# Performance work log

Hardware: AMD Instinct MI355X
Metric: run time of the kernel (lower is better)

Reference implementation:

```python
import jax, jax.numpy as jnp
import numpy as np

N, E, C = 50000, 10000, 500
NNZ = 400000
IN_DIM, EDGE_DIM, NODE_DIM, COMP_DIM = 128, 128, 128, 128


def _glorot(key, shape):
    fan = shape[0] + shape[1]
    return jax.random.normal(key, shape, jnp.float32) * (2.0 / fan) ** 0.5


def _seg_mean(vals, idx, num):
    # mean aggregation over segments (scatter-add + count normalize)
    s = jax.ops.segment_sum(vals, idx, num_segments=num)
    cnt = jax.ops.segment_sum(jnp.ones((idx.shape[0], 1), vals.dtype), idx, num_segments=num)
    return s / jnp.maximum(cnt, 1.0)


def _prelu(v, a):
    return jnp.where(v >= 0, v, a * v)


def _conv(x, ni, ei, ec_e, ec_c, nc_n, nc_c, n_nodes, n_edges, n_comps,
          Wne, Wen, Wec, Wnc, a):
    # node -> hyperedge message passing
    e = _seg_mean((x @ Wne)[ni], ei, n_edges)            # [E, edge_dim]
    e_act = _prelu(e, a)
    # hyperedge -> node
    n = _seg_mean((e_act @ Wen)[ei], ni, n_nodes)        # [N, node_dim]
    # edge -> component and node -> component
    c = _seg_mean((e_act @ Wec)[ec_e], ec_c, n_comps) + \
        _seg_mean((x @ Wnc)[nc_n], nc_c, n_comps)        # [C, comp_dim]
    return n, e, c


def setup_inputs() -> dict:
    key = jax.random.key(0)
    ks = jax.random.split(key, 16)
    x = jax.random.normal(ks[0], (N, IN_DIM), jnp.float32)
    hyperedge_index = jnp.stack([
        jax.random.randint(ks[1], (NNZ,), 0, N),
        jax.random.randint(ks[2], (NNZ,), 0, E),
    ])
    hyperedge_component_index = jnp.stack([
        jnp.arange(E), jax.random.randint(ks[3], (E,), 0, C)])
    node_component_index = jnp.stack([
        jnp.arange(N), jax.random.randint(ks[4], (N,), 0, C)])
    return dict(
        x=x,
        hyperedge_index=hyperedge_index,
        hyperedge_component_index=hyperedge_component_index,
        node_component_index=node_component_index,
        num_nodes=N, num_edges=E, num_components=C,
        W_ne0=_glorot(ks[5], (IN_DIM, EDGE_DIM)),
        W_en0=_glorot(ks[6], (EDGE_DIM, NODE_DIM)),
        W_ec0=_glorot(ks[7], (EDGE_DIM, COMP_DIM)),
        W_nc0=_glorot(ks[8], (IN_DIM, COMP_DIM)),
        W_ne1=_glorot(ks[9], (NODE_DIM, EDGE_DIM)),
        W_en1=_glorot(ks[10], (EDGE_DIM, NODE_DIM)),
        W_ec1=_glorot(ks[11], (EDGE_DIM, COMP_DIM)),
        W_nc1=_glorot(ks[12], (NODE_DIM, COMP_DIM)),
        prelu_a=jnp.array(0.25, jnp.float32),
    )


def reference(x, hyperedge_index, hyperedge_component_index, node_component_index,
              num_nodes, num_edges, num_components,
              W_ne0, W_en0, W_ec0, W_nc0, W_ne1, W_en1, W_ec1, W_nc1, prelu_a):
    ni, ei = hyperedge_index[0], hyperedge_index[1]
    ec_e, ec_c = hyperedge_component_index[0], hyperedge_component_index[1]
    nc_n, nc_c = node_component_index[0], node_component_index[1]
    layers = [(W_ne0, W_en0, W_ec0, W_nc0), (W_ne1, W_en1, W_ec1, W_nc1)]
    e_out = c_out = None
    for Wne, Wen, Wec, Wnc in layers:
        n_out, e_out, c_out = _conv(x, ni, ei, ec_e, ec_c, nc_n, nc_c,
                                    num_nodes, num_edges, num_components,
                                    Wne, Wen, Wec, Wnc, prelu_a)
        x = _prelu(n_out, prelu_a)  # HyperEncoder applies act between/after layers
    return (x, e_out, c_out)
```

## Files before the change

### kernel.cpp

```cpp
#include <hip/hip_runtime.h>
#include <stdint.h>

typedef unsigned int u32;
typedef _Float16 f16;
typedef f16 half8 __attribute__((ext_vector_type(8)));
typedef float f32x4 __attribute__((ext_vector_type(4)));
#define TS 4096
#define KB2 256
#define CH 2048

__device__ __forceinline__ float bflo(u32 u) { return __uint_as_float(u << 16); }
__device__ __forceinline__ float bfhi(u32 u) { return __uint_as_float(u & 0xffff0000u); }
__device__ __forceinline__ u32 f2bf(float x) {
    u32 u = __float_as_uint(x);
    return (u + 0x7fffu + ((u >> 16) & 1u)) >> 16;
}
__device__ __forceinline__ u32 pack2(float a, float b) { return f2bf(a) | (f2bf(b) << 16); }

__device__ __forceinline__ int bstart2(int b, int total) {
    return (int)(((unsigned long long)b * (u32)total + KB2 - 1) / KB2);
}

__device__ __forceinline__ int blk_exscan(int v, int& total) {
    __shared__ int ws[5];
    int t = threadIdx.x, lane = t & 63, w = t >> 6;
    int inc = v;
    for (int d = 1; d < 64; d <<= 1) { int u = __shfl_up(inc, d, 64); if (lane >= d) inc += u; }
    __syncthreads();
    if (lane == 63) ws[w] = inc;
    __syncthreads();
    if (t == 0) { int acc = 0; for (int i = 0; i < 4; ++i) { int x = ws[i]; ws[i] = acc; acc += x; } ws[4] = acc; }
    __syncthreads();
    total = ws[4];
    return ws[w] + (inc - v);
}

#define ACC8(v) do { \
    a[0] += bflo((v).x); a[1] += bfhi((v).x); a[2] += bflo((v).y); a[3] += bfhi((v).y); \
    a[4] += bflo((v).z); a[5] += bfhi((v).z); a[6] += bflo((v).w); a[7] += bfhi((v).w); } while (0)

__device__ __forceinline__ void seg_mean8(const u32* __restrict__ in,
                                          const int* __restrict__ items,
                                          const int* __restrict__ off,
                                          int nseg, int nrows, int seg, float a[8]) {
    int lane = threadIdx.x & 63;
    int rs = lane >> 4;
    int cc = lane & 15;
#pragma unroll
    for (int i = 0; i < 8; ++i) a[i] = 0.f;
    int s0 = 0, s1 = 0;
    if (seg < nseg) { s0 = off[seg]; s1 = off[seg + 1]; }
    const uint4* rows = (const uint4*)in;
    int base = s0;
    for (; base + 16 <= s1; base += 16) {
        u32 r0 = (u32)items[base + rs];
        u32 r1 = (u32)items[base + 4 + rs];
        u32 r2 = (u32)items[base + 8 + rs];
        u32 r3 = (u32)items[base + 12 + rs];
        r0 = (r0 < (u32)nrows) ? r0 : 0u;
        r1 = (r1 < (u32)nrows) ? r1 : 0u;
        r2 = (r2 < (u32)nrows) ? r2 : 0u;
        r3 = (r3 < (u32)nrows) ? r3 : 0u;
        uint4 v0 = rows[(size_t)r0 * 16 + cc];
        uint4 v1 = rows[(size_t)r1 * 16 + cc];
        uint4 v2 = rows[(size_t)r2 * 16 + cc];
        uint4 v3 = rows[(size_t)r3 * 16 + cc];
        ACC8(v0); ACC8(v1); ACC8(v2); ACC8(v3);
    }
    for (; base + 8 <= s1; base += 8) {
        u32 r0 = (u32)items[base + rs];
        u32 r1 = (u32)items[base + 4 + rs];
        r0 = (r0 < (u32)nrows) ? r0 : 0u;
        r1 = (r1 < (u32)nrows) ? r1 : 0u;
        uint4 v0 = rows[(size_t)r0 * 16 + cc];
        uint4 v1 = rows[(size_t)r1 * 16 + cc];
        ACC8(v0); ACC8(v1);
    }
    int idx = base + rs;
    if (idx < s1) {
        u32 r = (u32)items[idx]; r = (r < (u32)nrows) ? r : 0u;
        uint4 v = rows[(size_t)r * 16 + cc];
        ACC8(v);
    }
    idx += 4;
    if (idx < s1) {
        u32 r = (u32)items[idx]; r = (r < (u32)nrows) ? r : 0u;
        uint4 v = rows[(size_t)r * 16 + cc];
        ACC8(v);
    }
#pragma unroll
    for (int i = 0; i < 8; ++i) {
        a[i] += __shfl_xor(a[i], 16, 64);
        a[i] += __shfl_xor(a[i], 32, 64);
    }
    float inv = 1.f / fmaxf((float)(s1 - s0), 1.f);
#pragma unroll
    for (int i = 0; i < 8; ++i) a[i] *= inv;
}

__device__ __forceinline__ void agg4_body(const u32* __restrict__ in,
                                          const int* __restrict__ items,
                                          const int* __restrict__ off,
                                          float* __restrict__ out_f32,
                                          u32* __restrict__ out_bf,
                                          int nseg, int nrows, int do_prelu,
                                          const float* __restrict__ alpha_p, int seg) {
    if (seg >= nseg) return;
    int lane = threadIdx.x & 63;
    int rs = lane >> 4;
    int cc = lane & 15;
    float a[8];
    seg_mean8(in, items, off, nseg, nrows, seg, a);
    if (do_prelu) {
        float al = *alpha_p;
#pragma unroll
        for (int i = 0; i < 8; ++i) a[i] = (a[i] >= 0.f) ? a[i] : al * a[i];
    }
    if (rs == 0) {
        if (out_f32) {
            float* o = out_f32 + ((size_t)seg << 7) + cc * 8;
            *(float4*)o       = make_float4(a[0], a[1], a[2], a[3]);
            *(float4*)(o + 4) = make_float4(a[4], a[5], a[6], a[7]);
        }
        if (out_bf) {
            uint4 pk;
            pk.x = pack2(a[0], a[1]); pk.y = pack2(a[2], a[3]);
            pk.z = pack2(a[4], a[5]); pk.w = pack2(a[6], a[7]);
            *(uint4*)(out_bf + ((size_t)seg << 6) + cc * 4) = pk;
        }
    }
}

__global__ __launch_bounds__(256) void k_front(
        const int* __restrict__ ni, const int* __restrict__ ei,
        const int* __restrict__ nc_c, const int* __restrict__ ec_c,
        int* __restrict__ bcntE, int* __restrict__ bcntN,
        int* __restrict__ cnt_cn, int* __restrict__ cnt_ce,
        int nnz, int n, int e, int nbh,
        int* __restrict__ ticket,
        int* __restrict__ basesE, int* __restrict__ basesN,
        int* __restrict__ bcur_e, int* __restrict__ bcur_n,
        int* __restrict__ off_cn, int* __restrict__ off_ce,
        int* __restrict__ cur_cn, int* __restrict__ cur_ce, int c,
        const float* __restrict__ W0, const float* __restrict__ W1,
        const float* __restrict__ W2, const float* __restrict__ W3,
        const float* __restrict__ W4, const float* __restrict__ W5,
        f16* __restrict__ wt6) {
    int t = threadIdx.x;
    int b = blockIdx.x;
    if (b >= nbh) {
        int gid = (b - nbh) * 256 + t;
        if (gid >= 6 * 2048) return;
        int m = gid >> 11;
        int rem = gid & 2047;
        int cq = rem >> 4;
        int s = rem & 15;
        const float* W = (m == 0) ? W0 : (m == 1) ? W1 : (m == 2) ? W2 :
                         (m == 3) ? W3 : (m == 4) ? W4 : W5;
        int khi = ((s & 7) ^ (cq & 7)) | (s & 8);
        int k0 = khi << 3;
        union { f16 h[8]; uint4 v; } u;
#pragma unroll
        for (int j = 0; j < 8; ++j) u.h[j] = (f16)W[((k0 + j) << 7) + cq];
        *(uint4*)(wt6 + ((size_t)m << 14) + (cq << 7) + (s << 3)) = u.v;
        return;
    }
    __shared__ int hE[KB2], hN[KB2];
    __shared__ int lastflag;
    hE[t] = 0; hN[t] = 0;
    __syncthreads();
    int base = b * CH;
    int lim = base + CH; if (lim > nnz) lim = nnz;
    for (int i = base + t; i < lim; i += 256) {
        u32 v = (u32)ni[i], eg = (u32)ei[i];
        if (v >= (u32)n) v = 0;
        if (eg >= (u32)e) eg = 0;
        atomicAdd(&hE[(int)(((unsigned long long)eg * KB2) / (u32)e)], 1);
        atomicAdd(&hN[(int)(((unsigned long long)v  * KB2) / (u32)n)], 1);
    }
    __syncthreads();
    if (hE[t]) atomicAdd(&bcntE[t], hE[t]);
    if (hN[t]) atomicAdd(&bcntN[t], hN[t]);
    int gid = b * 256 + t, stride = nbh * 256;
    for (int j = gid; j < n + e; j += stride) {
        if (j < n) atomicAdd(&cnt_cn[nc_c[j]], 1);
        else       atomicAdd(&cnt_ce[ec_c[j - n]], 1);
    }
    __syncthreads();
    if (t == 0) {
        __threadfence();
        lastflag = (atomicAdd(ticket, 1) == nbh - 1);
    }
    __syncthreads();
    if (!lastflag) return;
    __threadfence();
    int tot;
    int v = bcntE[t];
    int ex = blk_exscan(v, tot);
    basesE[t] = ex; bcur_e[t] = ex;
    if (t == 0) basesE[KB2] = tot;
    v = bcntN[t];
    ex = blk_exscan(v, tot);
    basesN[t] = ex; bcur_n[t] = ex;
    if (t == 0) basesN[KB2] = tot;
    int i0 = 2 * t, i1 = 2 * t + 1;
    int v0 = (i0 < c) ? cnt_cn[i0] : 0;
    int v1 = (i1 < c) ? cnt_cn[i1] : 0;
    ex = blk_exscan(v0 + v1, tot);
    if (i0 < c) { off_cn[i0] = ex;      cur_cn[i0] = ex; }
    if (i1 < c) { off_cn[i1] = ex + v0; cur_cn[i1] = ex + v0; }
    if (t == 0) off_cn[c] = tot;
    v0 = (i0 < c) ? cnt_ce[i0] : 0;
    v1 = (i1 < c) ? cnt_ce[i1] : 0;
    ex = blk_exscan(v0 + v1, tot);
    if (i0 < c) { off_ce[i0] = ex;      cur_ce[i0] = ex; }
    if (i1 < c) { off_ce[i1] = ex + v0; cur_ce[i1] = ex + v0; }
    if (t == 0) off_ce[c] = tot;
}

__global__ __launch_bounds__(256) void k_part_a(
        const int* __restrict__ ni, const int* __restrict__ ei,
        int* __restrict__ bcur_e, int* __restrict__ bcur_n,
        u32* __restrict__ stg_e, u32* __restrict__ stg_n,
        const int* __restrict__ nc_n, const int* __restrict__ nc_c,
        const int* __restrict__ ec_e, const int* __restrict__ ec_c,
        int* __restrict__ cur_cn, int* __restrict__ cur_ce,
        int* __restrict__ csr_cn, int* __restrict__ csr_ce,
        const float2* __restrict__ xin, u32* __restrict__ xout, int npairs,
        int nnz, int n, int e, int nbh) {
    __shared__ u32 pk[CH];
    __shared__ unsigned short bb[CH];
    __shared__ int hist[KB2];
    __shared__ int gb[KB2];
    int t = threadIdx.x;
    int bx = blockIdx.x;
    if (bx >= 2 * nbh) {
        int j = (bx - 2 * nbh) * 256 + t;
        if (j < npairs) { float2 v = xin[j]; xout[j] = pack2(v.x, v.y); }
        return;
    }
    int side = bx >= nbh;
    int pb = side ? bx - nbh : bx;
    int base = pb * CH;
    int cnt  = nnz - base; if (cnt > CH) cnt = CH;
    for (int i = t; i < KB2; i += 256) hist[i] = 0;
    __syncthreads();
    u32 total = side ? (u32)n : (u32)e;
    for (int i = t; i < cnt; i += 256) {
        int v = ni[base + i], eg = ei[base + i];
        u32 key = side ? (u32)v : (u32)eg;
        u32 pay = side ? (u32)eg : (u32)v;
        if (key >= total) key = 0;
        u32 b = (u32)(((unsigned long long)key * KB2) / total);
        pk[i] = side ? (pay | (key << 14)) : (pay | (key << 16));
        bb[i] = (unsigned short)b;
        atomicAdd(&hist[b], 1);
    }
    __syncthreads();
    int* cursor = side ? bcur_n : bcur_e;
    u32* stg    = side ? stg_n  : stg_e;
    if (t < KB2) {
        int h = hist[t];
        gb[t] = h ? atomicAdd(&cursor[t], h) : 0;
        hist[t] = 0;
    }
    __syncthreads();
    for (int i = t; i < cnt; i += 256) {
        int b = bb[i];
        int r = atomicAdd(&hist[b], 1);
        stg[gb[b] + r] = pk[i];
    }
    int gid = pb * 256 + t;
    int stride = nbh * 256;
    if (side == 0) {
        for (int j = gid; j < e; j += stride) { int c = ec_c[j]; csr_ce[atomicAdd(&cur_ce[c], 1)] = ec_e[j]; }
    } else {
        for (int j = gid; j < n; j += stride) { int c = nc_c[j]; csr_cn[atomicAdd(&cur_cn[c], 1)] = nc_n[j]; }
    }
}

__global__ __launch_bounds__(256) void k_part_b2(
        const u32* __restrict__ stg_e, const u32* __restrict__ stg_n,
        const int* __restrict__ basesE, const int* __restrict__ basesN,
        int* __restrict__ off_e, int* __restrict__ off_n,
        int* __restrict__ csr_e, int* __restrict__ csr_n, int e, int n) {
    __shared__ int lcnt[256];
    int b = blockIdx.x, t = threadIdx.x;
    const u32* stg; const int* bases; int* off; int* csr; int total; int shift; u32 mask;
    if (b < KB2) { stg = stg_e; bases = basesE; off = off_e; csr = csr_e; total = e; shift = 16; mask = 0xFFFFu; }
    else { b -= KB2; stg = stg_n; bases = basesN; off = off_n; csr = csr_n; total = n; shift = 14; mask = 0x3FFFu; }
    int lo = bstart2(b, total), hi = bstart2(b + 1, total);
    int nid = hi - lo;
    int sbase = bases[b], send = bases[b + 1];
    lcnt[t] = 0;
    __syncthreads();
    for (int i = sbase + t; i < send; i += 256) {
        int key = (int)(stg[i] >> shift);
        atomicAdd(&lcnt[key - lo], 1);
    }
    __syncthreads();
    int cval = (t < nid) ? lcnt[t] : 0;
    int tot;
    int ex = blk_exscan(cval, tot);
    int cursor = sbase + ex;
    if (t < nid) { off[lo + t] = cursor; lcnt[t] = cursor; }
    if (t == 0 && hi == total) off[total] = send;
    __syncthreads();
    for (int i = sbase + t; i < send; i += 256) {
        u32 s = stg[i];
        int key = (int)(s >> shift);
        int pay = (int)(s & mask);
        int p = atomicAdd(&lcnt[key - lo], 1);
        csr[p] = pay;
    }
}

__global__ void k_cvt(const float2* __restrict__ in, u32* __restrict__ out, int npairs) {
    int j = blockIdx.x * blockDim.x + threadIdx.x;
    if (j < npairs) { float2 v = in[j]; out[j] = pack2(v.x, v.y); }
}

__global__ void k_hist_fb(const int* __restrict__ ni, const int* __restrict__ ei,
                          const int* __restrict__ nc_c, const int* __restrict__ ec_c,
                          int* __restrict__ deg_e, int* __restrict__ deg_n,
                          int* __restrict__ cnt_cn, int* __restrict__ cnt_ce,
                          int nnz, int n, int e) {
    int j = blockIdx.x * blockDim.x + threadIdx.x;
    if (j < nnz) {
        atomicAdd(&deg_e[ei[j]], 1);
        atomicAdd(&deg_n[ni[j]], 1);
    }
    if (j < n) atomicAdd(&cnt_cn[nc_c[j]], 1);
    if (j < e) atomicAdd(&cnt_ce[ec_c[j]], 1);
}

__device__ __forceinline__ void scan_sel(int b, int t0, int t01, int t012,
        const int* c0, int* o0, int* u0, int n0,
        const int* c1, int* o1, int* u1, int n1,
        const int* c2, int* o2, int* u2, int n2,
        const int* c3, int* o3, int* u3, int n3,
        const int*& cnt, int*& off, int*& cur, int& n, int& tile) {
    if (b < t0)        { cnt = c0; off = o0; cur = u0; n = n0; tile = b; }
    else if (b < t01)  { cnt = c1; off = o1; cur = u1; n = n1; tile = b - t0; }
    else if (b < t012) { cnt = c2; off = o2; cur = u2; n = n2; tile = b - t01; }
    else               { cnt = c3; off = o3; cur = u3; n = n3; tile = b - t012; }
}

__global__ void k_scan_p1(const int* c0, int n0, const int* c1, int n1,
                          const int* c2, int n2, const int* c3, int n3,
                          int t0, int t01, int t012, int* __restrict__ tilesum) {
    __shared__ int ws[4];
    int b = blockIdx.x;
    const int* cnt; int* off; int* cur; int n; int tile;
    scan_sel(b, t0, t01, t012, c0, nullptr, nullptr, n0, c1, nullptr, nullptr, n1,
             c2, nullptr, nullptr, n2, c3, nullptr, nullptr, n3, cnt, off, cur, n, tile);
    int base = tile * TS + threadIdx.x * 16;
    int s = 0;
#pragma unroll
    for (int i = 0; i < 16; ++i) { int idx = base + i; if (idx < n) s += cnt[idx]; }
    for (int d = 32; d; d >>= 1) s += __shfl_xor(s, d, 64);
    int lane = threadIdx.x & 63, w = threadIdx.x >> 6;
    if (lane == 0) ws[w] = s;
    __syncthreads();
    if (threadIdx.x == 0) tilesum[b] = ws[0] + ws[1] + ws[2] + ws[3];
}

__global__ void k_scan_p2(const int* __restrict__ tilesum, int* __restrict__ tilebase,
                          int t0, int t01, int t012, int t0123,
                          int* o0, int n0, int* o1, int n1, int* o2, int n2, int* o3, int n3) {
    if (threadIdx.x != 0 || blockIdx.x != 0) return;
    int carry = 0;
    for (int b = 0;    b < t0;    ++b) { tilebase[b] = carry; carry += tilesum[b]; } o0[n0] = carry;
    carry = 0;
    for (int b = t0;   b < t01;   ++b) { tilebase[b] = carry; carry += tilesum[b]; } o1[n1] = carry;
    carry = 0;
    for (int b = t01;  b < t012;  ++b) { tilebase[b] = carry; carry += tilesum[b]; } o2[n2] = carry;
    carry = 0;
    for (int b = t012; b < t0123; ++b) { tilebase[b] = carry; carry += tilesum[b]; } o3[n3] = carry;
}

__global__ void k_scan_p3(const int* c0, int* o0, int* u0, int n0,
                          const int* c1, int* o1, int* u1, int n1,
                          const int* c2, int* o2, int* u2, int n2,
                          const int* c3, int* o3, int* u3, int n3,
                          int t0, int t01, int t012, const int* __restrict__ tilebase) {
    __shared__ int wsum[4];
    int b = blockIdx.x;
    const int* cnt; int* off; int* cur; int n; int tile;
    scan_sel(b, t0, t01, t012, c0, o0, u0, n0, c1, o1, u1, n1,
             c2, o2, u2, n2, c3, o3, u3, n3, cnt, off, cur, n, tile);
    int lane = threadIdx.x & 63, w = threadIdx.x >> 6;
    int base = tile * TS + threadIdx.x * 16;
    int vals[16];
    int s = 0;
#pragma unroll
    for (int i = 0; i < 16; ++i) { int idx = base + i; int v = (idx < n) ? cnt[idx] : 0; vals[i] = v; s += v; }
    int inc = s;
    for (int d = 1; d < 64; d <<= 1) { int u = __shfl_up(inc, d, 64); if (lane >= d) inc += u; }
    if (lane == 63) wsum[w] = inc;
    __syncthreads();
    if (threadIdx.x == 0) {
        int acc = tilebase[b];
        for (int i = 0; i < 4; ++i) { int t = wsum[i]; wsum[i] = acc; acc += t; }
    }
    __syncthreads();
    int ex = wsum[w] + (inc - s);
#pragma unroll
    for (int i = 0; i < 16; ++i) {
        int idx = base + i;
        if (idx < n) { off[idx] = ex; cur[idx] = ex; }
        ex += vals[i];
    }
}

__global__ void k_scatter(const int* __restrict__ ni, const int* __restrict__ ei,
                          const int* __restrict__ nc_n, const int* __restrict__ nc_c,
                          const int* __restrict__ ec_e, const int* __restrict__ ec_c,
                          int* __restrict__ cur_e, int* __restrict__ cur_n,
                          int* __restrict__ cur_cn, int* __restrict__ cur_ce,
                          int* __restrict__ csr_e, int* __restrict__ csr_n,
                          int* __restrict__ csr_cn, int* __restrict__ csr_ce,
                          int nnz, int n, int e) {
    int j = blockIdx.x * blockDim.x + threadIdx.x;
    if (j < nnz) {
        int v = ni[j], eg = ei[j];
        csr_e[atomicAdd(&cur_e[eg], 1)] = v;
        csr_n[atomicAdd(&cur_n[v], 1)] = eg;
    }
    if (j < n) { int c = nc_c[j]; csr_cn[atomicAdd(&cur_cn[c], 1)] = nc_n[j]; }
    if (j < e) { int c = ec_c[j]; csr_ce[atomicAdd(&cur_ce[c], 1)] = ec_e[j]; }
}

__global__ __launch_bounds__(256) void k_agg4(
        const u32* __restrict__ in, const int* __restrict__ items,
        const int* __restrict__ off, float* __restrict__ out_f32,
        u32* __restrict__ out_bf,
        int nseg, int nrows, int do_prelu, const float* __restrict__ alpha_p) {
    int seg = blockIdx.x * (blockDim.x >> 6) + (threadIdx.x >> 6);
    agg4_body(in, items, off, out_f32, out_bf, nseg, nrows, do_prelu, alpha_p, seg);
}

__global__ __launch_bounds__(256) void k_agg4h(
        const u32* __restrict__ in, const int* __restrict__ items,
        const int* __restrict__ off, f16* __restrict__ outh,
        int nseg, int nrows) {
    int seg = blockIdx.x * (blockDim.x >> 6) + (threadIdx.x >> 6);
    if (seg >= nseg) return;
    float a[8];
    seg_mean8(in, items, off, nseg, nrows, seg, a);
    int lane = threadIdx.x & 63, rs = lane >> 4, cc = lane & 15;
    if (rs == 0) {
        union { f16 h[8]; uint4 v; } u;
#pragma unroll
        for (int i = 0; i < 8; ++i) u.h[i] = (f16)a[i];
        *(uint4*)(outh + ((size_t)seg << 7) + cc * 8) = u.v;
    }
}

__global__ __launch_bounds__(256) void k_agg_final(
        const u32* __restrict__ ybf, const int* __restrict__ csr_n, const int* __restrict__ off_n,
        float* __restrict__ out_x, int n, int e,
        const u32* __restrict__ eactbf, const int* __restrict__ csr_ce, const int* __restrict__ off_ce,
        float* __restrict__ ca_e,
        const u32* __restrict__ x1bf, const int* __restrict__ csr_cn, const int* __restrict__ off_cn,
        float* __restrict__ ca_n,
        int c, int nblkN, int ncb, const float* __restrict__ alpha_p) {
    int b = blockIdx.x;
    int wv = threadIdx.x >> 6;
    if (b < nblkN) {
        agg4_body(ybf, csr_n, off_n, out_x, nullptr, n, e, 1, alpha_p, b * 4 + wv);
    } else if (b < nblkN + ncb) {
        agg4_body(eactbf, csr_ce, off_ce, ca_e, nullptr, c, e, 0, nullptr, (b - nblkN) * 4 + wv);
    } else {
        agg4_body(x1bf, csr_cn, off_cn, ca_n, nullptr, c, n, 0, nullptr, (b - nblkN - ncb) * 4 + wv);
    }
}

__global__ __launch_bounds__(256) void k_mlp_mfma(
        const f16* __restrict__ Ah,
        const f16* __restrict__ W1t, const f16* __restrict__ W2t,
        float* __restrict__ out_raw, u32* __restrict__ out_actbf,
        u32* __restrict__ out_ybf, int M, const float* __restrict__ alpha_p) {
    __shared__ f16 As[32 * 128];
    __shared__ f16 Wt[128 * 128];
    int t = threadIdx.x;
    int rb = blockIdx.x * 32;
    float al = *alpha_p;
    {
        const uint4* src = (const uint4*)W1t;
        uint4* dst = (uint4*)Wt;
        for (int i = t; i < 2048; i += 256) dst[i] = src[i];
    }
    {
        const uint4* Ag = (const uint4*)Ah;
        for (int i = t; i < 512; i += 256) {
            int r = i >> 4, s = i & 15;
            int row = rb + r;
            uint4 v = make_uint4(0u, 0u, 0u, 0u);
            if (row < M) v = Ag[(size_t)row * 16 + s];
            *(uint4*)((char*)As + (r << 8) + ((s << 4) ^ ((r & 7) << 4))) = v;
        }
    }
    __syncthreads();

    int lane = t & 63, wv = t >> 6;
    int r0  = (wv >> 1) << 4;
    int ctb = (wv & 1) << 2;
    int frow = lane & 15;
    int fk = (lane >> 4) << 3;
    int rl0 = r0 + ((lane >> 4) << 2);
    int ar = r0 + frow;
    int asw = (ar & 7) << 4;

    f32x4 acc[4] = {{0.f,0.f,0.f,0.f},{0.f,0.f,0.f,0.f},{0.f,0.f,0.f,0.f},{0.f,0.f,0.f,0.f}};
#pragma unroll
    for (int ks = 0; ks < 4; ++ks) {
        int kb2 = (ks * 32 + fk) << 1;
        half8 a = *(const half8*)((const char*)As + (ar << 8) + (kb2 ^ asw));
#pragma unroll
        for (int j = 0; j < 4; ++j) {
            int c = ((ctb + j) << 4) + frow;
            half8 b = *(const half8*)((const char*)Wt + (c << 8) + (kb2 ^ ((c & 7) << 4)));
            acc[j] = __builtin_amdgcn_mfma_f32_16x16x32_f16(a, b, acc[j], 0, 0, 0);
        }
    }
    __syncthreads();
    {
        const uint4* src = (const uint4*)W2t;
        uint4* dst = (uint4*)Wt;
        for (int i = t; i < 2048; i += 256) dst[i] = src[i];
    }
#pragma unroll
    for (int j = 0; j < 4; ++j) {
        int c = ((ctb + j) << 4) + frow;
#pragma unroll
        for (int rg = 0; rg < 4; ++rg) {
            int rl = rl0 + rg;
            int row = rb + rl;
            float ev = acc[j][rg];
            if (out_raw != nullptr && row < M) out_raw[((size_t)row << 7) + c] = ev;
            float av = (ev >= 0.f) ? ev : al * ev;
            float po = __shfl_xor(av, 1, 64);
            if (out_actbf != nullptr && (frow & 1) == 0 && row < M)
                out_actbf[((size_t)row << 6) + (c >> 1)] = pack2(av, po);
            *(f16*)((char*)As + (rl << 8) + (((c << 1)) ^ ((rl & 7) << 4))) = (f16)av;
        }
    }
    __syncthreads();
    f32x4 acc2[4] = {{0.f,0.f,0.f,0.f},{0.f,0.f,0.f,0.f},{0.f,0.f,0.f,0.f},{0.f,0.f,0.f,0.f}};
#pragma unroll
    for (int ks = 0; ks < 4; ++ks) {
        int kb2 = (ks * 32 + fk) << 1;
        half8 a = *(const half8*)((const char*)As + (ar << 8) + (kb2 ^ asw));
#pragma unroll
        for (int j = 0; j < 4; ++j) {
            int c = ((ctb + j) << 4) + frow;
            half8 b = *(const half8*)((const char*)Wt + (c << 8) + (kb2 ^ ((c & 7) << 4)));
            acc2[j] = __builtin_amdgcn_mfma_f32_16x16x32_f16(a, b, acc2[j], 0, 0, 0);
        }
    }
#pragma unroll
    for (int j = 0; j < 4; ++j) {
        int c = ((ctb + j) << 4) + frow;
#pragma unroll
        for (int rg = 0; rg < 4; ++rg) {
            int rl = rl0 + rg;
            int row = rb + rl;
            float yv = acc2[j][rg];
            float po = __shfl_xor(yv, 1, 64);
            if ((frow & 1) == 0 && row < M)
                out_ybf[((size_t)row << 6) + (c >> 1)] = pack2(yv, po);
        }
    }
}

__global__ __launch_bounds__(256) void k_gemm_mfma(
        const float* __restrict__ A1, const f16* __restrict__ W1t,
        const float* __restrict__ A2, const f16* __restrict__ W2t,
        float* __restrict__ out, int M) {
    __shared__ f16 Asd[2][32 * 128];
    __shared__ f16 Wt[128 * 128];
    int t = threadIdx.x;
    int rb = blockIdx.x * 32;
    {
        const uint4* src = (const uint4*)W1t;
        uint4* dst = (uint4*)Wt;
        for (int i = t; i < 2048; i += 256) dst[i] = src[i];
    }
    for (int p = 0; p < 2; ++p) {
        const float* Ap = p ? A2 : A1;
        for (int i = t; i < 32 * 32; i += 256) {
            int r = i >> 5, dc = i & 31;
            int row = rb + r;
            float4 v = make_float4(0.f, 0.f, 0.f, 0.f);
            if (row < M) v = *(const float4*)(Ap + ((size_t)row << 7) + dc * 4);
            f16* q = (f16*)((char*)Asd[p] + (r << 8) + ((dc << 3) ^ ((r & 7) << 4)));
            q[0] = (f16)v.x; q[1] = (f16)v.y; q[2] = (f16)v.z; q[3] = (f16)v.w;
        }
    }
    __syncthreads();

    int lane = t & 63, wv = t >> 6;
    int r0  = (wv >> 1) << 4;
    int ctb = (wv & 1) << 2;
    int frow = lane & 15;
    int fk = (lane >> 4) << 3;
    int rl0 = r0 + ((lane >> 4) << 2);
    int ar = r0 + frow;
    int asw = (ar & 7) << 4;

    f32x4 acc[4] = {{0.f,0.f,0.f,0.f},{0.f,0.f,0.f,0.f},{0.f,0.f,0.f,0.f},{0.f,0.f,0.f,0.f}};
#pragma unroll
    for (int ks = 0; ks < 4; ++ks) {
        int kb2 = (ks * 32 + fk) << 1;
        half8 a = *(const half8*)((const char*)Asd[0] + (ar << 8) + (kb2 ^ asw));
#pragma unroll
        for (int j = 0; j < 4; ++j) {
            int c = ((ctb + j) << 4) + frow;
            half8 b = *(const half8*)((const char*)Wt + (c << 8) + (kb2 ^ ((c & 7) << 4)));
            acc[j] = __builtin_amdgcn_mfma_f32_16x16x32_f16(a, b, acc[j], 0, 0, 0);
        }
    }
    __syncthreads();
    {
        const uint4* src = (const uint4*)W2t;
        uint4* dst = (uint4*)Wt;
        for (int i = t; i < 2048; i += 256) dst[i] = src[i];
    }
    __syncthreads();
#pragma unroll
    for (int ks = 0; ks < 4; ++ks) {
        int kb2 = (ks * 32 + fk) << 1;
        half8 a = *(const half8*)((const char*)Asd[1] + (ar << 8) + (kb2 ^ asw));
#pragma unroll
        for (int j = 0; j < 4; ++j) {
            int c = ((ctb + j) << 4) + frow;
            half8 b = *(const half8*)((const char*)Wt + (c << 8) + (kb2 ^ ((c & 7) << 4)));
            acc[j] = __builtin_amdgcn_mfma_f32_16x16x32_f16(a, b, acc[j], 0, 0, 0);
        }
    }
#pragma unroll
    for (int j = 0; j < 4; ++j) {
        int c = ((ctb + j) << 4) + frow;
#pragma unroll
        for (int rg = 0; rg < 4; ++rg) {
            int row = rb + rl0 + rg;
            if (row < M) out[((size_t)row << 7) + c] = acc[j][rg];
        }
    }
}

extern "C" void kernel_launch(void* const* d_in, const int* in_sizes, int n_in,
                              void* d_out, int out_size, void* d_ws, size_t ws_size,
                              hipStream_t stream) {
    const int N   = in_sizes[0] / 128;
    const int NNZ = in_sizes[1] / 2;
    const int E   = in_sizes[2] / 2;
    const int C   = 500;

    const float* x0 = (const float*)d_in[0];
    const int* ni   = (const int*)d_in[1];
    const int* ei   = ni + NNZ;
    const int* ec_e = (const int*)d_in[2];
    const int* ec_c = ec_e + E;
    const int* nc_n = (const int*)d_in[3];
    const int* nc_c = nc_n + N;
    const float* Wne0 = (const float*)d_in[7];
    const float* Wen0 = (const float*)d_in[8];
    const float* Wne1 = (const float*)d_in[11];
    const float* Wen1 = (const float*)d_in[12];
    const float* Wec1 = (const float*)d_in[13];
    const float* Wnc1 = (const float*)d_in[14];
    const float* alpha = (const float*)d_in[15];

    float* out_x = (float*)d_out;
    float* out_e = out_x + (size_t)N * 128;
    float* out_c = out_e + (size_t)E * 128;

    char* w = (char*)d_ws;
    auto alloc = [&](size_t bytes) { char* p = w; w += (bytes + 255) & ~(size_t)255; return p; };
    int* zgrp   = (int*)alloc((size_t)(2 * KB2 + 2 * C + 1) * 4);
    int* bcntE  = zgrp;
    int* bcntN  = zgrp + KB2;
    int* cnt_cn = zgrp + 2 * KB2;
    int* cnt_ce = zgrp + 2 * KB2 + C;
    int* ticket = zgrp + 2 * KB2 + 2 * C;
    int* off_e  = (int*)alloc((size_t)(E + 1) * 4);
    int* off_n  = (int*)alloc((size_t)(N + 1) * 4);
    int* off_cn = (int*)alloc((size_t)(C + 1) * 4);
    int* off_ce = (int*)alloc((size_t)(C + 1) * 4);
    int* cur_cn = (int*)alloc((size_t)C * 4);
    int* cur_ce = (int*)alloc((size_t)C * 4);
    int* csr_e  = (int*)alloc((size_t)NNZ * 4);
    int* csr_n  = (int*)alloc((size_t)NNZ * 4);
    int* csr_cn = (int*)alloc((size_t)N * 4);
    int* csr_ce = (int*)alloc((size_t)E * 4);
    int* basesE = (int*)alloc((size_t)(KB2 + 1) * 4);
    int* basesN = (int*)alloc((size_t)(KB2 + 1) * 4);
    int* bcur_e = (int*)alloc(KB2 * 4);
    int* bcur_n = (int*)alloc(KB2 * 4);
    u32* stg_e  = (u32*)alloc((size_t)NNZ * 4);
    u32* stg_n  = (u32*)alloc((size_t)NNZ * 4);
    u32* xbf    = (u32*)alloc((size_t)N * 64 * 4);
    u32* x1bf   = (u32*)alloc((size_t)N * 64 * 4);
    u32* ybf    = (u32*)alloc((size_t)E * 64 * 4);
    u32* eactbf = (u32*)alloc((size_t)E * 64 * 4);
    f16* xah    = (f16*)alloc((size_t)E * 128 * 2);
    float* ca_e = (float*)alloc((size_t)C * 128 * 4);
    float* ca_n = (float*)alloc((size_t)C * 128 * 4);
    f16* wt6    = (f16*)alloc((size_t)6 * 16384 * 2);
    int* deg_e    = (int*)alloc((size_t)E * 4);
    int* deg_n    = (int*)alloc((size_t)N * 4);
    int* cur_e    = (int*)alloc((size_t)E * 4);
    int* cur_n    = (int*)alloc((size_t)N * 4);
    int* tilesum  = (int*)alloc(64 * 4);
    int* tilebase = (int*)alloc(64 * 4);

    const int th = 256;
    const int npairs = N * 64;
    const int nbh = (NNZ + CH - 1) / CH;
    const int nkc = (npairs + th - 1) / th;

    bool binned = (E <= 16384) && (N <= 65536) && (E >= KB2) && (N >= KB2) &&
                  ((N + KB2 - 1) / KB2 <= 256) && (C <= 512);
    const int nbh_eff = binned ? nbh : 0;

    hipMemsetAsync(zgrp, 0, (size_t)(2 * KB2 + 2 * C + 1) * 4, stream);
    k_front<<<nbh_eff + 48, 256, 0, stream>>>(
        ni, ei, nc_c, ec_c,
        bcntE, bcntN, cnt_cn, cnt_ce, NNZ, N, E, nbh_eff,
        ticket, basesE, basesN, bcur_e, bcur_n,
        off_cn, off_ce, cur_cn, cur_ce, C,
        Wne0, Wen0, Wne1, Wen1, Wec1, Wnc1, wt6);

    if (binned) {
        k_part_a<<<2 * nbh + nkc, 256, 0, stream>>>(
            ni, ei, bcur_e, bcur_n, stg_e, stg_n,
            nc_n, nc_c, ec_e, ec_c,
            cur_cn, cur_ce, csr_cn, csr_ce,
            (const float2*)x0, xbf, npairs, NNZ, N, E, nbh);
        k_part_b2<<<2 * KB2, 256, 0, stream>>>(stg_e, stg_n, basesE, basesN,
                                               off_e, off_n, csr_e, csr_n, E, N);
    } else {
        hipMemsetAsync(deg_e, 0, (size_t)E * 4, stream);
        hipMemsetAsync(deg_n, 0, (size_t)N * 4, stream);
        k_cvt<<<(npairs + th - 1) / th, th, 0, stream>>>((const float2*)x0, xbf, npairs);
        k_hist_fb<<<(NNZ > N + E ? NNZ : N + E) / th + 1, th, 0, stream>>>(
            ni, ei, nc_c, ec_c, deg_e, deg_n, cnt_cn, cnt_ce, NNZ, N, E);
        const int t0 = (E + TS - 1) / TS, t1 = (N + TS - 1) / TS;
        const int t2 = (C + TS - 1) / TS, t3 = (C + TS - 1) / TS;
        const int t01 = t0 + t1, t012 = t01 + t2, t0123 = t012 + t3;
        k_scan_p1<<<t0123, 256, 0, stream>>>(deg_e, E, deg_n, N, cnt_cn, C, cnt_ce, C,
                                             t0, t01, t012, tilesum);
        k_scan_p2<<<1, 64, 0, stream>>>(tilesum, tilebase, t0, t01, t012, t0123,
                                        off_e, E, off_n, N, off_cn, C, off_ce, C);
        k_scan_p3<<<t0123, 256, 0, stream>>>(deg_e, off_e, cur_e, E,
                                             deg_n, off_n, cur_n, N,
                                             cnt_cn, off_cn, cur_cn, C,
                                             cnt_ce, off_ce, cur_ce, C,
                                             t0, t01, t012, tilebase);
        k_scatter<<<(NNZ + th - 1) / th, th, 0, stream>>>(ni, ei, nc_n, nc_c, ec_e, ec_c,
                                                          cur_e, cur_n, cur_cn, cur_ce,
                                                          csr_e, csr_n, csr_cn, csr_ce, NNZ, N, E);
    }

    const int gmlp = (E + 31) / 32;
    k_agg4h<<<(E + 3) / 4, 256, 0, stream>>>(xbf, csr_e, off_e, xah, E, N);
    k_mlp_mfma<<<gmlp, 256, 0, stream>>>(xah, wt6, wt6 + 16384, nullptr, nullptr, ybf, E, alpha);
    k_agg4<<<(N + 3) / 4, 256, 0, stream>>>(ybf, csr_n, off_n, nullptr, x1bf, N, E, 1, alpha);
    k_agg4h<<<(E + 3) / 4, 256, 0, stream>>>(x1bf, csr_e, off_e, xah, E, N);
    k_mlp_mfma<<<gmlp, 256, 0, stream>>>(xah, wt6 + 2 * 16384, wt6 + 3 * 16384,
                                         out_e, eactbf, ybf, E, alpha);
    {
        const int nblkN = (N + 3) / 4;
        const int ncb   = (C + 3) / 4;
        k_agg_final<<<nblkN + 2 * ncb, 256, 0, stream>>>(
            ybf, csr_n, off_n, out_x, N, E,
            eactbf, csr_ce, off_ce, ca_e,
            x1bf,   csr_cn, off_cn, ca_n,
            C, nblkN, ncb, alpha);
    }
    k_gemm_mfma<<<(C + 31) / 32, 256, 0, stream>>>(ca_e, wt6 + 4 * 16384,
                                                   ca_n, wt6 + 5 * 16384, out_c, C);
}
```

Baseline: 263.2 us.

## Overlap component aggregation with MLP and split final comp GEMM

Moves the node-to-component mean aggregation into extra blocks of the second MLP kernel, and computes the ca_n @ Wnc GEMM inside the final aggregation kernel. A small follow-up kernel then accumulates ca_e @ Wec into out_c. Two extra unswizzled fp16 weight copies are prepared for the register-direct GEMM body. Non-temporal stores are used for the large fp32 outputs. The aim is to hide the small component work under larger kernels. The cost is a read-modify-write on out_c and an ordering dependency between the two GEMM halves.

```diff
diff --git a/kernel.cpp b/kernel.cpp
--- a/kernel.cpp
+++ b/kernel.cpp
@@ -104,7 +104,8 @@
                                           float* __restrict__ out_f32,
                                           u32* __restrict__ out_bf,
                                           int nseg, int nrows, int do_prelu,
-                                          const float* __restrict__ alpha_p, int seg) {
+                                          const float* __restrict__ alpha_p, int seg,
+                                          int nt) {
     if (seg >= nseg) return;
     int lane = threadIdx.x & 63;
     int rs = lane >> 4;
@@ -119,14 +120,91 @@
     if (rs == 0) {
         if (out_f32) {
             float* o = out_f32 + ((size_t)seg << 7) + cc * 8;
-            *(float4*)o       = make_float4(a[0], a[1], a[2], a[3]);
-            *(float4*)(o + 4) = make_float4(a[4], a[5], a[6], a[7]);
+            f32x4 v0 = {a[0], a[1], a[2], a[3]};
+            f32x4 v1 = {a[4], a[5], a[6], a[7]};
+            if (nt) {
+                __builtin_nontemporal_store(v0, (f32x4*)o);
+                __builtin_nontemporal_store(v1, (f32x4*)(o + 4));
+            } else {
+                *(f32x4*)o = v0;
+                *(f32x4*)(o + 4) = v1;
+            }
         }
         if (out_bf) {
             uint4 pk;
             pk.x = pack2(a[0], a[1]); pk.y = pack2(a[2], a[3]);
             pk.z = pack2(a[4], a[5]); pk.w = pack2(a[6], a[7]);
             *(uint4*)(out_bf + ((size_t)seg << 6) + cc * 4) = pk;
+        }
+    }
+}
+
+__device__ __forceinline__ void aggh_body(const u32* __restrict__ in,
+                                          const int* __restrict__ items,
+                                          const int* __restrict__ off,
+                                          f16* __restrict__ outh,
+                                          int nseg, int nrows, int seg) {
+    if (seg >= nseg) return;
+    float a[8];
+    seg_mean8(in, items, off, nseg, nrows, seg, a);
+    int lane = threadIdx.x & 63, rs = lane >> 4, cc = lane & 15;
+    if (rs == 0) {
+        union { f16 h[8]; uint4 v; } u;
+#pragma unroll
+        for (int i = 0; i < 8; ++i) u.h[i] = (f16)a[i];
+        *(uint4*)(outh + ((size_t)seg << 7) + cc * 8) = u.v;
+    }
+}
+
+__device__ __forceinline__ void gemm1_body(const float* __restrict__ A,
+                                           const f16* __restrict__ WL,
+                                           float* __restrict__ out, int M,
+                                           int rb, int accum, int nt) {
+    int t = threadIdx.x, lane = t & 63, wv = t >> 6;
+    int r0 = (wv >> 1) << 4, ctb = (wv & 1) << 2;
+    int frow = lane & 15, fk = (lane >> 4) << 3;
+    int rl0 = r0 + ((lane >> 4) << 2);
+    int ar = rb + r0 + frow;
+    f32x4 acc[4];
+#pragma unroll
+    for (int j = 0; j < 4; ++j) {
+        int c = ((ctb + j) << 4) + frow;
+#pragma unroll
+        for (int rg = 0; rg < 4; ++rg) {
+            int row = rb + rl0 + rg;
+            acc[j][rg] = (accum && row < M) ? out[((size_t)row << 7) + c] : 0.f;
+        }
+    }
+#pragma unroll
+    for (int ks = 0; ks < 4; ++ks) {
+        int kb = ks * 32 + fk;
+        half8 af;
+        if (ar < M) {
+            float4 a0 = *(const float4*)(A + ((size_t)ar << 7) + kb);
+            float4 a1 = *(const float4*)(A + ((size_t)ar << 7) + kb + 4);
+            af[0] = (f16)a0.x; af[1] = (f16)a0.y; af[2] = (f16)a0.z; af[3] = (f16)a0.w;
+            af[4] = (f16)a1.x; af[5] = (f16)a1.y; af[6] = (f16)a1.z; af[7] = (f16)a1.w;
+        } else {
+#pragma unroll
+            for (int j = 0; j < 8; ++j) af[j] = (f16)0.f;
+        }
+#pragma unroll
+        for (int j = 0; j < 4; ++j) {
+            int c = ((ctb + j) << 4) + frow;
+            half8 bf = *(const half8*)(WL + ((size_t)c << 7) + kb);
+            acc[j] = __builtin_amdgcn_mfma_f32_16x16x32_f16(af, bf, acc[j], 0, 0, 0);
+        }
+    }
+#pragma unroll
+    for (int j = 0; j < 4; ++j) {
+        int c = ((ctb + j) << 4) + frow;
+#pragma unroll
+        for (int rg = 0; rg < 4; ++rg) {
+            int row = rb + rl0 + rg;
+            if (row < M) {
+                if (nt) __builtin_nontemporal_store(acc[j][rg], out + ((size_t)row << 7) + c);
+                else out[((size_t)row << 7) + c] = acc[j][rg];
+            }
         }
     }
 }
@@ -150,14 +228,15 @@
     int b = blockIdx.x;
     if (b >= nbh) {
         int gid = (b - nbh) * 256 + t;
-        if (gid >= 6 * 2048) return;
+        if (gid >= 8 * 2048) return;
         int m = gid >> 11;
         int rem = gid & 2047;
         int cq = rem >> 4;
         int s = rem & 15;
         const float* W = (m == 0) ? W0 : (m == 1) ? W1 : (m == 2) ? W2 :
-                         (m == 3) ? W3 : (m == 4) ? W4 : W5;
-        int khi = ((s & 7) ^ (cq & 7)) | (s & 8);
+                         (m == 3) ? W3 : (m == 4) ? W4 : (m == 5) ? W5 :
+                         (m == 6) ? W4 : W5;
+        int khi = (m < 6) ? (((s & 7) ^ (cq & 7)) | (s & 8)) : s;
         int k0 = khi << 3;
         union { f16 h[8]; uint4 v; } u;
 #pragma unroll
@@ -437,7 +516,7 @@
         u32* __restrict__ out_bf,
         int nseg, int nrows, int do_prelu, const float* __restrict__ alpha_p) {
     int seg = blockIdx.x * (blockDim.x >> 6) + (threadIdx.x >> 6);
-    agg4_body(in, items, off, out_f32, out_bf, nseg, nrows, do_prelu, alpha_p, seg);
+    agg4_body(in, items, off, out_f32, out_bf, nseg, nrows, do_prelu, alpha_p, seg, 0);
 }
 
 __global__ __launch_bounds__(256) void k_agg4h(
@@ -445,16 +524,7 @@
         const int* __restrict__ off, f16* __restrict__ outh,
         int nseg, int nrows) {
     int seg = blockIdx.x * (blockDim.x >> 6) + (threadIdx.x >> 6);
-    if (seg >= nseg) return;
-    float a[8];
-    seg_mean8(in, items, off, nseg, nrows, seg, a);
-    int lane = threadIdx.x & 63, rs = lane >> 4, cc = lane & 15;
-    if (rs == 0) {
-        union { f16 h[8]; uint4 v; } u;
-#pragma unroll
-        for (int i = 0; i < 8; ++i) u.h[i] = (f16)a[i];
-        *(uint4*)(outh + ((size_t)seg << 7) + cc * 8) = u.v;
-    }
+    aggh_body(in, items, off, outh, nseg, nrows, seg);
 }
 
 __global__ __launch_bounds__(256) void k_agg_final(
@@ -462,28 +532,45 @@
         float* __restrict__ out_x, int n, int e,
         const u32* __restrict__ eactbf, const int* __restrict__ csr_ce, const int* __restrict__ off_ce,
         float* __restrict__ ca_e,
-        const u32* __restrict__ x1bf, const int* __restrict__ csr_cn, const int* __restrict__ off_cn,
-        float* __restrict__ ca_n,
+        const float* __restrict__ ca_n, const f16* __restrict__ WncL,
+        float* __restrict__ out_c,
         int c, int nblkN, int ncb, const float* __restrict__ alpha_p) {
     int b = blockIdx.x;
     int wv = threadIdx.x >> 6;
     if (b < nblkN) {
-        agg4_body(ybf, csr_n, off_n, out_x, nullptr, n, e, 1, alpha_p, b * 4 + wv);
+        agg4_body(ybf, csr_n, off_n, out_x, nullptr, n, e, 1, alpha_p, b * 4 + wv, 1);
     } else if (b < nblkN + ncb) {
-        agg4_body(eactbf, csr_ce, off_ce, ca_e, nullptr, c, e, 0, nullptr, (b - nblkN) * 4 + wv);
+        agg4_body(eactbf, csr_ce, off_ce, ca_e, nullptr, c, e, 0, nullptr, (b - nblkN) * 4 + wv, 0);
     } else {
-        agg4_body(x1bf, csr_cn, off_cn, ca_n, nullptr, c, n, 0, nullptr, (b - nblkN - ncb) * 4 + wv);
-    }
+        gemm1_body(ca_n, WncL, out_c, c, (b - nblkN - ncb) * 32, 0, 0);
+    }
+}
+
+__global__ __launch_bounds__(256) void k_gemm1(
+        const float* __restrict__ A, const f16* __restrict__ WL,
+        float* __restrict__ out, int M) {
+    gemm1_body(A, WL, out, M, blockIdx.x * 32, 1, 1);
 }
 
 __global__ __launch_bounds__(256) void k_mlp_mfma(
         const f16* __restrict__ Ah,
         const f16* __restrict__ W1t, const f16* __restrict__ W2t,
         float* __restrict__ out_raw, u32* __restrict__ out_actbf,
-        u32* __restrict__ out_ybf, int M, const float* __restrict__ alpha_p) {
+        u32* __restrict__ out_ybf, int M, const float* __restrict__ alpha_p,
+        int nmlp,
+        const u32* __restrict__ cn_in, const int* __restrict__ cn_items,
+        const int* __restrict__ cn_off, float* __restrict__ cn_out,
+        int cn_nseg, int cn_nrows) {
     __shared__ f16 As[32 * 128];
     __shared__ f16 Wt[128 * 128];
     int t = threadIdx.x;
+    if (blockIdx.x >= nmlp) {
+        if (cn_out == nullptr) return;
+        int seg = (blockIdx.x - nmlp) * 4 + (t >> 6);
+        agg4_body(cn_in, cn_items, cn_off, cn_out, nullptr, cn_nseg, cn_nrows, 0,
+                  alpha_p, seg, 0);
+        return;
+    }
     int rb = blockIdx.x * 32;
     float al = *alpha_p;
     {
@@ -538,7 +625,8 @@
             int rl = rl0 + rg;
             int row = rb + rl;
             float ev = acc[j][rg];
-            if (out_raw != nullptr && row < M) out_raw[((size_t)row << 7) + c] = ev;
+            if (out_raw != nullptr && row < M)
+                __builtin_nontemporal_store(ev, out_raw + ((size_t)row << 7) + c);
             float av = (ev >= 0.f) ? ev : al * ev;
             float po = __shfl_xor(av, 1, 64);
             if (out_actbf != nullptr && (frow & 1) == 0 && row < M)
@@ -570,82 +658,6 @@
             float po = __shfl_xor(yv, 1, 64);
             if ((frow & 1) == 0 && row < M)
                 out_ybf[((size_t)row << 6) + (c >> 1)] = pack2(yv, po);
-        }
-    }
-}
-
-__global__ __launch_bounds__(256) void k_gemm_mfma(
-        const float* __restrict__ A1, const f16* __restrict__ W1t,
-        const float* __restrict__ A2, const f16* __restrict__ W2t,
-        float* __restrict__ out, int M) {
-    __shared__ f16 Asd[2][32 * 128];
-    __shared__ f16 Wt[128 * 128];
-    int t = threadIdx.x;
-    int rb = blockIdx.x * 32;
-    {
-        const uint4* src = (const uint4*)W1t;
-        uint4* dst = (uint4*)Wt;
-        for (int i = t; i < 2048; i += 256) dst[i] = src[i];
-    }
-    for (int p = 0; p < 2; ++p) {
-        const float* Ap = p ? A2 : A1;
-        for (int i = t; i < 32 * 32; i += 256) {
-            int r = i >> 5, dc = i & 31;
-            int row = rb + r;
-            float4 v = make_float4(0.f, 0.f, 0.f, 0.f);
-            if (row < M) v = *(const float4*)(Ap + ((size_t)row << 7) + dc * 4);
-            f16* q = (f16*)((char*)Asd[p] + (r << 8) + ((dc << 3) ^ ((r & 7) << 4)));
-            q[0] = (f16)v.x; q[1] = (f16)v.y; q[2] = (f16)v.z; q[3] = (f16)v.w;
-        }
-    }
-    __syncthreads();
-
-    int lane = t & 63, wv = t >> 6;
-    int r0  = (wv >> 1) << 4;
-    int ctb = (wv & 1) << 2;
-    int frow = lane & 15;
-    int fk = (lane >> 4) << 3;
-    int rl0 = r0 + ((lane >> 4) << 2);
-    int ar = r0 + frow;
-    int asw = (ar & 7) << 4;
-
-    f32x4 acc[4] = {{0.f,0.f,0.f,0.f},{0.f,0.f,0.f,0.f},{0.f,0.f,0.f,0.f},{0.f,0.f,0.f,0.f}};
-#pragma unroll
-    for (int ks = 0; ks < 4; ++ks) {
-        int kb2 = (ks * 32 + fk) << 1;
-        half8 a = *(const half8*)((const char*)Asd[0] + (ar << 8) + (kb2 ^ asw));
-#pragma unroll
-        for (int j = 0; j < 4; ++j) {
-            int c = ((ctb + j) << 4) + frow;
-            half8 b = *(const half8*)((const char*)Wt + (c << 8) + (kb2 ^ ((c & 7) << 4)));
-            acc[j] = __builtin_amdgcn_mfma_f32_16x16x32_f16(a, b, acc[j], 0, 0, 0);
-        }
-    }
-    __syncthreads();
-    {
-        const uint4* src = (const uint4*)W2t;
-        uint4* dst = (uint4*)Wt;
-        for (int i = t; i < 2048; i += 256) dst[i] = src[i];
-    }
-    __syncthreads();
-#pragma unroll
-    for (int ks = 0; ks < 4; ++ks) {
-        int kb2 = (ks * 32 + fk) << 1;
-        half8 a = *(const half8*)((const char*)Asd[1] + (ar << 8) + (kb2 ^ asw));
-#pragma unroll
-        for (int j = 0; j < 4; ++j) {
-            int c = ((ctb + j) << 4) + frow;
-            half8 b = *(const half8*)((const char*)Wt + (c << 8) + (kb2 ^ ((c & 7) << 4)));
-            acc[j] = __builtin_amdgcn_mfma_f32_16x16x32_f16(a, b, acc[j], 0, 0, 0);
-        }
-    }
-#pragma unroll
-    for (int j = 0; j < 4; ++j) {
-        int c = ((ctb + j) << 4) + frow;
-#pragma unroll
-        for (int rg = 0; rg < 4; ++rg) {
-            int row = rb + rl0 + rg;
-            if (row < M) out[((size_t)row << 7) + c] = acc[j][rg];
         }
     }
 }
@@ -708,7 +720,7 @@
     f16* xah    = (f16*)alloc((size_t)E * 128 * 2);
     float* ca_e = (float*)alloc((size_t)C * 128 * 4);
     float* ca_n = (float*)alloc((size_t)C * 128 * 4);
-    f16* wt6    = (f16*)alloc((size_t)6 * 16384 * 2);
+    f16* wt6    = (f16*)alloc((size_t)8 * 16384 * 2);
     int* deg_e    = (int*)alloc((size_t)E * 4);
     int* deg_n    = (int*)alloc((size_t)N * 4);
     int* cur_e    = (int*)alloc((size_t)E * 4);
@@ -726,7 +738,7 @@
     const int nbh_eff = binned ? nbh : 0;
 
     hipMemsetAsync(zgrp, 0, (size_t)(2 * KB2 + 2 * C + 1) * 4, stream);
-    k_front<<<nbh_eff + 48, 256, 0, stream>>>(
+    k_front<<<nbh_eff + 64, 256, 0, stream>>>(
         ni, ei, nc_c, ec_c,
         bcntE, bcntN, cnt_cn, cnt_ce, NNZ, N, E, nbh_eff,
         ticket, basesE, basesN, bcur_e, bcur_n,
@@ -765,21 +777,24 @@
     }
 
     const int gmlp = (E + 31) / 32;
+    const int ncb  = (C + 3) / 4;
+    const int gc   = (C + 31) / 32;
     k_agg4h<<<(E + 3) / 4, 256, 0, stream>>>(xbf, csr_e, off_e, xah, E, N);
-    k_mlp_mfma<<<gmlp, 256, 0, stream>>>(xah, wt6, wt6 + 16384, nullptr, nullptr, ybf, E, alpha);
+    k_mlp_mfma<<<gmlp, 256, 0, stream>>>(xah, wt6, wt6 + 16384, nullptr, nullptr, ybf,
+                                         E, alpha, gmlp,
+                                         nullptr, nullptr, nullptr, nullptr, 0, 0);
     k_agg4<<<(N + 3) / 4, 256, 0, stream>>>(ybf, csr_n, off_n, nullptr, x1bf, N, E, 1, alpha);
     k_agg4h<<<(E + 3) / 4, 256, 0, stream>>>(x1bf, csr_e, off_e, xah, E, N);
-    k_mlp_mfma<<<gmlp, 256, 0, stream>>>(xah, wt6 + 2 * 16384, wt6 + 3 * 16384,
-                                         out_e, eactbf, ybf, E, alpha);
+    k_mlp_mfma<<<gmlp + ncb, 256, 0, stream>>>(xah, wt6 + 2 * 16384, wt6 + 3 * 16384,
+                                               out_e, eactbf, ybf, E, alpha, gmlp,
+                                               x1bf, csr_cn, off_cn, ca_n, C, N);
     {
         const int nblkN = (N + 3) / 4;
-        const int ncb   = (C + 3) / 4;
-        k_agg_final<<<nblkN + 2 * ncb, 256, 0, stream>>>(
+        k_agg_final<<<nblkN + ncb + gc, 256, 0, stream>>>(
             ybf, csr_n, off_n, out_x, N, E,
             eactbf, csr_ce, off_ce, ca_e,
-            x1bf,   csr_cn, off_cn, ca_n,
+            ca_n, wt6 + 7 * 16384, out_c,
             C, nblkN, ncb, alpha);
     }
-    k_gemm_mfma<<<(C + 31) / 32, 256, 0, stream>>>(ca_e, wt6 + 4 * 16384,
-                                                   ca_n, wt6 + 5 * 16384, out_c, C);
-}
+    k_gemm1<<<gc, 256, 0, stream>>>(ca_e, wt6 + 6 * 16384, out_c, C);
+}
```

After: 256.7 us, median of 2. 1.03x faster.
